# Kernel tuning notes

Measured on AMD Instinct MI355X. Metric: run time of the kernel, lower is better.

The kernel has to match this reference:

```python
import jax, jax.numpy as jnp
import numpy as np

N, E, F_IN, H, L, E_FEAT, G, OUT = 100000, 1600000, 8, 128, 4, 16, 256, 256


def setup_inputs() -> dict:
    key = jax.random.key(0)
    ks = jax.random.split(key, 12)
    inp = {
        "x": jax.random.normal(ks[0], (N, F_IN), jnp.float32),
        "edge_index": jax.random.randint(ks[1], (2, E), 0, N),
        "edge_attr": jax.random.uniform(ks[2], (E, E_FEAT), jnp.float32),
        "batch": jnp.sort(jax.random.randint(ks[3], (N,), 0, G)),
        "emb_W": jax.random.normal(ks[4], (F_IN, H), jnp.float32) / np.sqrt(F_IN),
        "emb_b": jnp.zeros((H,), jnp.float32),
        "edge_W": jax.random.normal(ks[5], (L, E_FEAT, H), jnp.float32) / np.sqrt(E_FEAT),
        "edge_b": jnp.zeros((L, H), jnp.float32),
        "nn_W": jax.random.normal(ks[6], (L, H, H), jnp.float32) / np.sqrt(H),
        "nn_b": jnp.zeros((L, H), jnp.float32),
        "bn_g": jnp.ones((L, H), jnp.float32),
        "bn_b": jnp.zeros((L, H), jnp.float32),
        "lin_W": jax.random.normal(ks[7], (H, OUT), jnp.float32) / np.sqrt(H),
        "lin_b": jnp.zeros((OUT,), jnp.float32),
    }
    return inp


def reference(x, edge_index, edge_attr, batch, emb_W, emb_b, edge_W, edge_b,
              nn_W, nn_b, bn_g, bn_b, lin_W, lin_b):
    eps_bn = 1e-5
    src, dst = edge_index[0], edge_index[1]
    h = x @ emb_W + emb_b  # node embedding [N,H]
    for l in range(L):
        e = edge_attr @ edge_W[l] + edge_b[l]          # [E,H] edge embedding
        msg = jax.nn.relu(h[src] + e)                   # gather + message
        agg = jax.ops.segment_sum(msg, dst, num_segments=N)  # scatter-add
        hc = (h + agg) @ nn_W[l] + nn_b[l]             # GINE nn (eps=0)
        mu = jnp.mean(hc, axis=0)
        var = jnp.mean((hc - mu) ** 2, axis=0)          # biased var (train BN)
        hc = (hc - mu) * jax.lax.rsqrt(var + eps_bn) * bn_g[l] + bn_b[l]
        hc = jax.nn.gelu(hc, approximate=False)
        h = h + hc                                      # 'res' residual
    out = h @ lin_W + lin_b                             # [N,OUT]
    rep = jax.ops.segment_sum(out, batch, num_segments=G)  # global_add_pool
    return rep
```

## Files before the change

kernel.cpp:

```cpp
#include <hip/hip_runtime.h>
#include <hip/hip_fp16.h>
#include <math.h>

#define GG 256

typedef __attribute__((ext_vector_type(8))) short short8;
typedef __attribute__((ext_vector_type(4))) float f32x4;
typedef _Float16 half4v __attribute__((ext_vector_type(4)));
typedef __attribute__((ext_vector_type(8))) unsigned uint8v;

__device__ __forceinline__ unsigned short f2bf(float x) {
  union { float f; unsigned u; } v; v.f = x;
  unsigned r = v.u + 0x7fff + ((v.u >> 16) & 1);
  return (unsigned short)(r >> 16);
}

__device__ __forceinline__ unsigned pack_h2(float a, float b) {
  __half2 h = __floats2half2_rn(a, b);
  return *(unsigned*)&h;
}

__device__ __forceinline__ uint8v sload8(const void* p) {
  uint8v r;
  asm volatile("s_load_dwordx8 %0, %1, 0x0"
               : "=s"(r) : "s"((unsigned long long)p));
  return r;
}
__device__ __forceinline__ void swait() {
  asm volatile("s_waitcnt lgkmcnt(0)" ::: "memory");
  __builtin_amdgcn_sched_barrier(0);
}

__global__ __launch_bounds__(256) void k_emb(const float* __restrict__ x,
    const float* __restrict__ W, const float* __restrict__ b,
    float* __restrict__ h, unsigned short* __restrict__ hb, int N) {
  int idx = blockIdx.x * 256 + threadIdx.x;
  if (idx >= N * 32) return;
  int n = idx >> 5, q = idx & 31;
  const float* xr = x + (size_t)n * 8;
  float xs[8];
#pragma unroll
  for (int k = 0; k < 8; ++k) xs[k] = xr[k];
  float4 acc = ((const float4*)b)[q];
#pragma unroll
  for (int k = 0; k < 8; ++k) {
    float4 w = ((const float4*)(W + (size_t)k * 128))[q];
    acc.x += xs[k] * w.x; acc.y += xs[k] * w.y;
    acc.z += xs[k] * w.z; acc.w += xs[k] * w.w;
  }
  ((float4*)h)[idx] = acc;
  ushort4 hv4 = make_ushort4(f2bf(acc.x), f2bf(acc.y), f2bf(acc.z), f2bf(acc.w));
  *(ushort4*)(hb + (size_t)idx * 4) = hv4;
}

__global__ __launch_bounds__(256) void k_wconv2(const float* __restrict__ eW,
    unsigned* __restrict__ eWf) {
  int i = blockIdx.x * 256 + threadIdx.x;
  if (i >= 2048) return;
  int lane = i & 63, nt = (i >> 6) & 7, l = i >> 9;
  int l15 = lane & 15, quad = lane >> 4;
  const float* base = eW + (size_t)l * 16 * 128 + (size_t)(nt * 16 + l15);
  unsigned lo = pack_h2(base[(quad * 4 + 0) * 128], base[(quad * 4 + 1) * 128]);
  unsigned hi = pack_h2(base[(quad * 4 + 2) * 128], base[(quad * 4 + 3) * 128]);
  eWf[(size_t)i * 2] = lo;
  eWf[(size_t)i * 2 + 1] = hi;
}

__global__ __launch_bounds__(256) void k_nnconv(const float* __restrict__ W,
    unsigned short* __restrict__ WT) {
  int i = blockIdx.x * 256 + threadIdx.x;
  if (i >= 4 * 128 * 128) return;
  int n = i & 127, k = (i >> 7) & 127, l = i >> 14;
  WT[((size_t)(l * 128 + n)) * 128 + k] = f2bf(W[i]);
}

__global__ void k_hist(const int* __restrict__ dst, int* __restrict__ deg, int E) {
  int e = blockIdx.x * blockDim.x + threadIdx.x;
  if (e < E) atomicAdd(&deg[dst[e]], 1);
}

__global__ __launch_bounds__(256) void k_scan_reduce(const int* __restrict__ deg,
    int* __restrict__ bsum, int N) {
  __shared__ int sd[256];
  int i = blockIdx.x * 256 + threadIdx.x;
  sd[threadIdx.x] = (i < N) ? deg[i] : 0;
  __syncthreads();
  for (int s = 128; s > 0; s >>= 1) {
    if (threadIdx.x < s) sd[threadIdx.x] += sd[threadIdx.x + s];
    __syncthreads();
  }
  if (threadIdx.x == 0) bsum[blockIdx.x] = sd[0];
}

__global__ __launch_bounds__(512) void k_scan_mid(int* bsum, int nb) {
  __shared__ int sd[512];
  int t = threadIdx.x;
  int v = (t < nb) ? bsum[t] : 0;
  sd[t] = v; __syncthreads();
  for (int d = 1; d < 512; d <<= 1) {
    int xv = (t >= d) ? sd[t - d] : 0;
    __syncthreads();
    sd[t] += xv;
    __syncthreads();
  }
  if (t < nb) bsum[t] = sd[t] - v;
}

__global__ __launch_bounds__(256) void k_scan_final(const int* __restrict__ deg,
    const int* __restrict__ bsum, int* __restrict__ offs,
    int* __restrict__ cursor, int N) {
  __shared__ int sd[256];
  int t = threadIdx.x;
  int i = blockIdx.x * 256 + t;
  int v = (i < N) ? deg[i] : 0;
  sd[t] = v; __syncthreads();
  for (int d = 1; d < 256; d <<= 1) {
    int xv = (t >= d) ? sd[t - d] : 0;
    __syncthreads();
    sd[t] += xv;
    __syncthreads();
  }
  int off = bsum[blockIdx.x] + sd[t] - v;
  if (i < N) {
    offs[i] = off; cursor[i] = off;
    if (i == N - 1) offs[N] = off + v;
  }
}

__global__ void k_fill(const int* __restrict__ src, const int* __restrict__ dst,
    const float* __restrict__ attr, int* __restrict__ cursor,
    int* __restrict__ csrc, uint4* __restrict__ cattr16, int E) {
  int e = blockIdx.x * blockDim.x + threadIdx.x;
  if (e >= E) return;
  int d = dst[e];
  int pos = atomicAdd(&cursor[d], 1);
  csrc[pos] = src[e];
  const float4* a = (const float4*)(attr + (size_t)e * 16);
  float4 a0 = a[0], a1 = a[1], a2 = a[2], a3 = a[3];
  uint4 o0, o1;
  o0.x = pack_h2(a0.x, a0.y); o0.y = pack_h2(a0.z, a0.w);
  o0.z = pack_h2(a1.x, a1.y); o0.w = pack_h2(a1.z, a1.w);
  o1.x = pack_h2(a2.x, a2.y); o1.y = pack_h2(a2.z, a2.w);
  o1.z = pack_h2(a3.x, a3.y); o1.w = pack_h2(a3.z, a3.w);
  cattr16[(size_t)pos * 2] = o0;
  cattr16[(size_t)pos * 2 + 1] = o1;
}

__global__ void k_gstart(const int* __restrict__ batch, int* __restrict__ gstart,
                         int N, int Gn) {
  int i = blockIdx.x * blockDim.x + threadIdx.x;
  if (i >= N) return;
  int b = batch[i];
  if (i == 0) { for (int g = 0; g <= b; ++g) gstart[g] = 0; }
  else { int bp = batch[i - 1]; for (int g = bp + 1; g <= b; ++g) gstart[g] = i; }
  if (i == N - 1) { for (int g = b + 1; g <= Gn; ++g) gstart[g] = N; }
}

__global__ __launch_bounds__(256) void k_edge_agg(const float* __restrict__ h,
    const unsigned* __restrict__ hb32,
    const uint4* __restrict__ cattr16, const int* __restrict__ csrc,
    const int* __restrict__ offs, const unsigned* __restrict__ eWf,
    const float* __restrict__ eb, unsigned* __restrict__ hpa16,
    float* __restrict__ cstats, int N) {
  __shared__ float elds_all[4][16 * 132];
  int t = threadIdx.x;
  if (blockIdx.x == 0) cstats[t] = 0.f;
  int lane = t & 63;
  int l15 = lane & 15, quad = lane >> 4;
  int wid = blockIdx.x * 4 + (t >> 6);
  int nw = gridDim.x * 4;
  float* elds = elds_all[t >> 6];
  uint2 bfr[8];
#pragma unroll
  for (int nt = 0; nt < 8; ++nt) bfr[nt] = ((const uint2*)eWf)[nt * 64 + lane];
  float2 bias = *(const float2*)(eb + 2 * lane);
  const unsigned* hb_l = hb32 + lane;

#define GI(r, SC)                                                           \
  unsigned u##r = 0;                                                        \
  if (j0 + (r) < je) u##r = hb_l[(size_t)(unsigned)(SC) * 64];

#define EPI(r, UU, AX, AY)                                                  \
  if (j0 + (r) < je) {                                                      \
    float2 ev = *(const float2*)&elds[(r) * 132 + 2 * lane];                \
    union { unsigned uu; float ff; } c0, c1;                                \
    c0.uu = (UU) << 16; c1.uu = (UU) & 0xffff0000u;                         \
    AX += fmaxf(ev.x + bias.x + c0.ff, 0.f);                                \
    AY += fmaxf(ev.y + bias.y + c1.ff, 0.f);                                \
  }

  for (int n = wid; n < N; n += nw) {
    int jb = __builtin_amdgcn_readfirstlane(offs[n]);
    int je = __builtin_amdgcn_readfirstlane(offs[n + 1]);
    float ax = 0.f, ay = 0.f, bx = 0.f, by = 0.f;
    for (int j0 = jb; j0 < je; j0 += 16) {
      uint8v scA = sload8((const char*)csrc + ((size_t)(unsigned)j0 << 2));
      uint8v scB = sload8((const char*)csrc + ((size_t)(unsigned)(j0 + 8) << 2));
      uint2 araw = *(const uint2*)((const char*)cattr16 +
                    ((size_t)(unsigned)(j0 + l15)) * 32 + quad * 8);
      swait();
      GI(0, scA[0]) GI(1, scA[1]) GI(2, scA[2]) GI(3, scA[3])
      GI(4, scA[4]) GI(5, scA[5]) GI(6, scA[6]) GI(7, scA[7])
      GI(8, scB[0]) GI(9, scB[1]) GI(10, scB[2]) GI(11, scB[3])
      GI(12, scB[4]) GI(13, scB[5]) GI(14, scB[6]) GI(15, scB[7])
      half4v av;
      __builtin_memcpy(&av, &araw, 8);
      f32x4 ee[8];
#pragma unroll
      for (int nt = 0; nt < 8; ++nt) {
        half4v bv;
        __builtin_memcpy(&bv, &bfr[nt], 8);
        ee[nt] = __builtin_amdgcn_mfma_f32_16x16x16f16(
            av, bv, (f32x4){0.f, 0.f, 0.f, 0.f}, 0, 0, 0);
      }
#pragma unroll
      for (int nt = 0; nt < 8; ++nt)
#pragma unroll
        for (int reg = 0; reg < 4; ++reg)
          elds[(quad * 4 + reg) * 132 + nt * 16 + l15] = ee[nt][reg];
      EPI(0, u0, ax, ay)  EPI(1, u1, bx, by)
      EPI(2, u2, ax, ay)  EPI(3, u3, bx, by)
      EPI(4, u4, ax, ay)  EPI(5, u5, bx, by)
      EPI(6, u6, ax, ay)  EPI(7, u7, bx, by)
      EPI(8, u8, ax, ay)  EPI(9, u9, bx, by)
      EPI(10, u10, ax, ay) EPI(11, u11, bx, by)
      EPI(12, u12, ax, ay) EPI(13, u13, bx, by)
      EPI(14, u14, ax, ay) EPI(15, u15, bx, by)
    }
    float2 hvv = *(const float2*)(h + (size_t)n * 128 + 2 * lane);
    float rx = hvv.x + ax + bx;
    float ry = hvv.y + ay + by;
    hpa16[(size_t)n * 64 + lane] = ((unsigned)f2bf(ry) << 16) | (unsigned)f2bf(rx);
  }
#undef GI
#undef EPI
}

__global__ __launch_bounds__(256) void k_gemm_mfma(
    const unsigned short* __restrict__ A16, const unsigned short* __restrict__ WT16,
    const float* __restrict__ bias, float* __restrict__ hc,
    float* __restrict__ cstats, int N) {
  __shared__ short a_lds[128 * 136];
  __shared__ short w_lds[128 * 136];
  int t = threadIdx.x;
  int rowbase = blockIdx.x * 128;
  {
    int r = t >> 1;
    int off = (t & 1) * 64;
    const short* ga = (const short*)A16 + (size_t)(rowbase + r) * 128 + off;
    short* la = &a_lds[r * 136 + off];
    const short* gw = (const short*)WT16 + (size_t)r * 128 + off;
    short* lw = &w_lds[r * 136 + off];
    if (rowbase + r < N) {
#pragma unroll
      for (int jj = 0; jj < 8; ++jj)
        *(uint4*)(la + jj * 8) = *(const uint4*)(ga + jj * 8);
    } else {
#pragma unroll
      for (int jj = 0; jj < 8; ++jj)
        *(uint4*)(la + jj * 8) = make_uint4(0, 0, 0, 0);
    }
#pragma unroll
    for (int jj = 0; jj < 8; ++jj)
      *(uint4*)(lw + jj * 8) = *(const uint4*)(gw + jj * 8);
  }
  __syncthreads();
  int w = t >> 6;
  int lane = t & 63;
  int l15 = lane & 15, quad = lane >> 4;
  f32x4 acc[2][8];
#pragma unroll
  for (int rt = 0; rt < 2; ++rt)
#pragma unroll
    for (int nt = 0; nt < 8; ++nt)
      acc[rt][nt] = (f32x4){0.f, 0.f, 0.f, 0.f};
#pragma unroll
  for (int kc = 0; kc < 4; ++kc) {
    int k0 = kc * 32 + quad * 8;
    short8 af0 = *(const short8*)&a_lds[(w * 32 + l15) * 136 + k0];
    short8 af1 = *(const short8*)&a_lds[(w * 32 + 16 + l15) * 136 + k0];
#pragma unroll
    for (int nt = 0; nt < 8; ++nt) {
      short8 bf = *(const short8*)&w_lds[(nt * 16 + l15) * 136 + k0];
      acc[0][nt] = __builtin_amdgcn_mfma_f32_16x16x32_bf16(af0, bf, acc[0][nt], 0, 0, 0);
      acc[1][nt] = __builtin_amdgcn_mfma_f32_16x16x32_bf16(af1, bf, acc[1][nt], 0, 0, 0);
    }
  }
  float sA[8], sQ[8];
#pragma unroll
  for (int nt = 0; nt < 8; ++nt) { sA[nt] = 0.f; sQ[nt] = 0.f; }
#pragma unroll
  for (int nt = 0; nt < 8; ++nt) {
    int col = nt * 16 + l15;
    float bv = bias[col];
#pragma unroll
    for (int rt = 0; rt < 2; ++rt) {
      int rbase = rowbase + w * 32 + rt * 16 + quad * 4;
#pragma unroll
      for (int reg = 0; reg < 4; ++reg) {
        int row = rbase + reg;
        float v = acc[rt][nt][reg] + bv;
        if (row < N) {
          hc[(size_t)row * 128 + col] = v;
          sA[nt] += v; sQ[nt] += v * v;
        }
      }
    }
  }
#pragma unroll
  for (int nt = 0; nt < 8; ++nt) {
    sA[nt] += __shfl_xor(sA[nt], 16);
    sA[nt] += __shfl_xor(sA[nt], 32);
    sQ[nt] += __shfl_xor(sQ[nt], 16);
    sQ[nt] += __shfl_xor(sQ[nt], 32);
  }
  __syncthreads();
  float* sdA = (float*)a_lds;
  float* sdQ = (float*)w_lds;
  if (quad == 0) {
#pragma unroll
    for (int nt = 0; nt < 8; ++nt) {
      sdA[w * 128 + nt * 16 + l15] = sA[nt];
      sdQ[w * 128 + nt * 16 + l15] = sQ[nt];
    }
  }
  __syncthreads();
  if (t < 128) {
    float s = sdA[t] + sdA[128 + t] + sdA[256 + t] + sdA[384 + t];
    float s2 = sdQ[t] + sdQ[128 + t] + sdQ[256 + t] + sdQ[384 + t];
    atomicAdd(&cstats[t], s);
    atomicAdd(&cstats[128 + t], s2);
  }
}

__global__ __launch_bounds__(256) void k_bn(const float* __restrict__ hc,
    const float* __restrict__ cstats,
    const float* __restrict__ g, const float* __restrict__ bb,
    float* __restrict__ h, unsigned short* __restrict__ hb, int N) {
  int idx = blockIdx.x * 256 + threadIdx.x;
  if (idx >= N * 32) return;
  int q = idx & 31;
  float invN = 1.f / (float)N;
  float4 cs = ((const float4*)cstats)[q];
  float4 cq = ((const float4*)cstats)[q + 32];
  float4 gv = ((const float4*)g)[q];
  float4 bv = ((const float4*)bb)[q];
  float4 v = ((const float4*)hc)[idx];
  float4 hv = ((const float4*)h)[idx];
#define BN1(X)                                                      \
  { float mu = cs.X * invN;                                         \
    float var = cq.X * invN - mu * mu;                              \
    float xn = (v.X - mu) * rsqrtf(var + 1e-5f) * gv.X + bv.X;      \
    hv.X += 0.5f * xn * (1.f + erff(xn * 0.70710678118654752f)); }
  BN1(x) BN1(y) BN1(z) BN1(w)
#undef BN1
  ((float4*)h)[idx] = hv;
  if (hb) {
    ushort4 hv4 = make_ushort4(f2bf(hv.x), f2bf(hv.y), f2bf(hv.z), f2bf(hv.w));
    *(ushort4*)(hb + (size_t)idx * 4) = hv4;
  }
}

__global__ __launch_bounds__(256) void k_poolfinal(const float* __restrict__ h,
    const int* __restrict__ gstart, const float* __restrict__ W,
    const float* __restrict__ b, float* __restrict__ out) {
  int g = blockIdx.x;
  int t = threadIdx.x, c = t & 127, half = t >> 7;
  int n0 = gstart[g], n1 = gstart[g + 1];
  float s = 0.f;
  for (int n = n0 + half; n < n1; n += 2) s += h[(size_t)n * 128 + c];
  __shared__ float ls[256];
  __shared__ float pr[128];
  ls[t] = s; __syncthreads();
  if (t < 128) pr[t] = ls[t] + ls[t + 128];
  __syncthreads();
  float cnt = (float)(n1 - n0);
  float acc = cnt * b[t];
#pragma unroll 8
  for (int k = 0; k < 128; ++k) acc += pr[k] * W[(size_t)k * 256 + t];
  out[(size_t)g * 256 + t] = acc;
}

extern "C" void kernel_launch(void* const* d_in, const int* in_sizes, int n_in,
                              void* d_out, int out_size, void* d_ws, size_t ws_size,
                              hipStream_t stream) {
  const float* x     = (const float*)d_in[0];
  const int*   eidx  = (const int*)d_in[1];
  const float* eattr = (const float*)d_in[2];
  const int*   batch = (const int*)d_in[3];
  const float* embW  = (const float*)d_in[4];
  const float* embB  = (const float*)d_in[5];
  const float* edgeW = (const float*)d_in[6];
  const float* edgeB = (const float*)d_in[7];
  const float* nnW   = (const float*)d_in[8];
  const float* nnB   = (const float*)d_in[9];
  const float* bnG   = (const float*)d_in[10];
  const float* bnB   = (const float*)d_in[11];
  const float* linW  = (const float*)d_in[12];
  const float* linB  = (const float*)d_in[13];
  float* out = (float*)d_out;

  int N = in_sizes[0] / 8;
  int E = in_sizes[1] / 2;
  const int* src = eidx;
  const int* dst = eidx + E;

  char* wptr = (char*)d_ws;
  auto alloc = [&](size_t bytes) {
    char* p = wptr; wptr += (bytes + 255) & ~(size_t)255; return p;
  };
  float* h      = (float*)alloc((size_t)N * 128 * 4);
  float* hc     = (float*)alloc((size_t)N * 128 * 4);
  unsigned short* hb = (unsigned short*)alloc((size_t)N * 128 * 2);
  unsigned* hpa16 = (unsigned*)alloc((size_t)N * 64 * 4);
  uint4* cattr16 = (uint4*)alloc((size_t)E * 32 + 1024);
  int*   csrc   = (int*)alloc((size_t)E * 4 + 256);
  int*   offs   = (int*)alloc((size_t)(N + 1) * 4);
  int*   cursor = (int*)alloc((size_t)N * 4);
  int*   deg    = (int*)alloc((size_t)N * 4);
  int nb = (N + 255) / 256;
  int*   bsum   = (int*)alloc((size_t)nb * 4);
  float* cstats = (float*)alloc(256 * 4);
  unsigned* eWf = (unsigned*)alloc(4096 * 4);
  unsigned short* WT16 = (unsigned short*)alloc(4 * 128 * 128 * 2);
  int*   gstart = (int*)alloc((size_t)(GG + 1) * 4);

  int q32 = (N * 32 + 255) / 256;

  hipMemsetAsync(deg, 0, (size_t)N * 4, stream);
  k_emb<<<q32, 256, 0, stream>>>(x, embW, embB, h, hb, N);
  k_wconv2<<<8, 256, 0, stream>>>(edgeW, eWf);
  k_nnconv<<<256, 256, 0, stream>>>(nnW, WT16);
  k_hist<<<(E + 255) / 256, 256, 0, stream>>>(dst, deg, E);
  k_scan_reduce<<<nb, 256, 0, stream>>>(deg, bsum, N);
  k_scan_mid<<<1, 512, 0, stream>>>(bsum, nb);
  k_scan_final<<<nb, 256, 0, stream>>>(deg, bsum, offs, cursor, N);
  k_fill<<<(E + 255) / 256, 256, 0, stream>>>(src, dst, eattr, cursor, csrc, cattr16, E);
  k_gstart<<<(N + 255) / 256, 256, 0, stream>>>(batch, gstart, N, GG);

  int gblk = (N + 127) / 128;
  for (int l = 0; l < 4; ++l) {
    k_edge_agg<<<8192, 256, 0, stream>>>(h, (const unsigned*)hb, cattr16, csrc,
        offs, eWf + (size_t)l * 1024, edgeB + (size_t)l * 128, hpa16, cstats, N);
    k_gemm_mfma<<<gblk, 256, 0, stream>>>((const unsigned short*)hpa16,
        WT16 + (size_t)l * 128 * 128, nnB + (size_t)l * 128, hc, cstats, N);
    k_bn<<<q32, 256, 0, stream>>>(hc, cstats,
        bnG + (size_t)l * 128, bnB + (size_t)l * 128, h, (l == 3) ? nullptr : hb, N);
  }
  k_poolfinal<<<GG, 256, 0, stream>>>(h, gstart, linW, linB, out);
}
```

Baseline: 1.064 ms.

## Prefetch next edge chunk indices and attrs; store edge embeddings as fp16 in LDS

Software-pipelines the per-node edge loop in the edge aggregation kernel. The scalar loads of the next 16 source indices and the next edge-attribute fragment are issued before the current chunk's MFMA and epilogue, so their latency overlaps with compute. It also halves the LDS staging of the MFMA edge embedding by storing fp16 instead of fp32. The cost is extra scalar registers and a loss of precision in the staged edge embeddings.

```diff
diff --git a/kernel.cpp b/kernel.cpp
--- a/kernel.cpp
+++ b/kernel.cpp
@@ -28,6 +28,10 @@
 }
 __device__ __forceinline__ void swait() {
   asm volatile("s_waitcnt lgkmcnt(0)" ::: "memory");
+  __builtin_amdgcn_sched_barrier(0);
+}
+__device__ __forceinline__ void swait2(uint8v& a, uint8v& b) {
+  asm volatile("s_waitcnt lgkmcnt(0)" : "+s"(a), "+s"(b) :: "memory");
   __builtin_amdgcn_sched_barrier(0);
 }
 
@@ -162,14 +166,14 @@
     const int* __restrict__ offs, const unsigned* __restrict__ eWf,
     const float* __restrict__ eb, unsigned* __restrict__ hpa16,
     float* __restrict__ cstats, int N) {
-  __shared__ float elds_all[4][16 * 132];
+  __shared__ __half elds_all[4][16 * 136];
   int t = threadIdx.x;
   if (blockIdx.x == 0) cstats[t] = 0.f;
   int lane = t & 63;
   int l15 = lane & 15, quad = lane >> 4;
   int wid = blockIdx.x * 4 + (t >> 6);
   int nw = gridDim.x * 4;
-  float* elds = elds_all[t >> 6];
+  __half* elds = elds_all[t >> 6];
   uint2 bfr[8];
 #pragma unroll
   for (int nt = 0; nt < 8; ++nt) bfr[nt] = ((const uint2*)eWf)[nt * 64 + lane];
@@ -182,50 +186,69 @@
 
 #define EPI(r, UU, AX, AY)                                                  \
   if (j0 + (r) < je) {                                                      \
-    float2 ev = *(const float2*)&elds[(r) * 132 + 2 * lane];                \
+    __half2 ev2 = *(__half2*)&elds[(r) * 136 + 2 * lane];                   \
     union { unsigned uu; float ff; } c0, c1;                                \
     c0.uu = (UU) << 16; c1.uu = (UU) & 0xffff0000u;                         \
-    AX += fmaxf(ev.x + bias.x + c0.ff, 0.f);                                \
-    AY += fmaxf(ev.y + bias.y + c1.ff, 0.f);                                \
-  }
+    AX += fmaxf(__low2float(ev2) + bias.x + c0.ff, 0.f);                    \
+    AY += fmaxf(__high2float(ev2) + bias.y + c1.ff, 0.f);                   \
+  }
+
+#define LOADA(DST, J0)                                                      \
+  DST = *(const uint2*)((const char*)cattr16 +                              \
+        ((size_t)(unsigned)((J0) + l15)) * 32 + quad * 8);
 
   for (int n = wid; n < N; n += nw) {
     int jb = __builtin_amdgcn_readfirstlane(offs[n]);
     int je = __builtin_amdgcn_readfirstlane(offs[n + 1]);
     float ax = 0.f, ay = 0.f, bx = 0.f, by = 0.f;
-    for (int j0 = jb; j0 < je; j0 += 16) {
-      uint8v scA = sload8((const char*)csrc + ((size_t)(unsigned)j0 << 2));
-      uint8v scB = sload8((const char*)csrc + ((size_t)(unsigned)(j0 + 8) << 2));
-      uint2 araw = *(const uint2*)((const char*)cattr16 +
-                    ((size_t)(unsigned)(j0 + l15)) * 32 + quad * 8);
-      swait();
-      GI(0, scA[0]) GI(1, scA[1]) GI(2, scA[2]) GI(3, scA[3])
-      GI(4, scA[4]) GI(5, scA[5]) GI(6, scA[6]) GI(7, scA[7])
-      GI(8, scB[0]) GI(9, scB[1]) GI(10, scB[2]) GI(11, scB[3])
-      GI(12, scB[4]) GI(13, scB[5]) GI(14, scB[6]) GI(15, scB[7])
-      half4v av;
-      __builtin_memcpy(&av, &araw, 8);
-      f32x4 ee[8];
-#pragma unroll
-      for (int nt = 0; nt < 8; ++nt) {
-        half4v bv;
-        __builtin_memcpy(&bv, &bfr[nt], 8);
-        ee[nt] = __builtin_amdgcn_mfma_f32_16x16x16f16(
-            av, bv, (f32x4){0.f, 0.f, 0.f, 0.f}, 0, 0, 0);
+    if (jb < je) {
+      uint8v scA = sload8((const char*)csrc + ((size_t)(unsigned)jb << 2));
+      uint8v scB = sload8((const char*)csrc + ((size_t)(unsigned)(jb + 8) << 2));
+      uint2 araw;
+      LOADA(araw, jb)
+      swait2(scA, scB);
+      for (int j0 = jb;;) {
+        GI(0, scA[0]) GI(1, scA[1]) GI(2, scA[2]) GI(3, scA[3])
+        GI(4, scA[4]) GI(5, scA[5]) GI(6, scA[6]) GI(7, scA[7])
+        GI(8, scB[0]) GI(9, scB[1]) GI(10, scB[2]) GI(11, scB[3])
+        GI(12, scB[4]) GI(13, scB[5]) GI(14, scB[6]) GI(15, scB[7])
+        bool more = (j0 + 16 < je);
+        uint8v scA2, scB2;
+        uint2 araw2;
+        if (more) {
+          scA2 = sload8((const char*)csrc + ((size_t)(unsigned)(j0 + 16) << 2));
+          scB2 = sload8((const char*)csrc + ((size_t)(unsigned)(j0 + 24) << 2));
+          LOADA(araw2, j0 + 16)
+        }
+        half4v av;
+        __builtin_memcpy(&av, &araw, 8);
+        f32x4 ee[8];
+#pragma unroll
+        for (int nt = 0; nt < 8; ++nt) {
+          half4v bv;
+          __builtin_memcpy(&bv, &bfr[nt], 8);
+          ee[nt] = __builtin_amdgcn_mfma_f32_16x16x16f16(
+              av, bv, (f32x4){0.f, 0.f, 0.f, 0.f}, 0, 0, 0);
+        }
+#pragma unroll
+        for (int nt = 0; nt < 8; ++nt)
+#pragma unroll
+          for (int reg = 0; reg < 4; ++reg)
+            elds[(quad * 4 + reg) * 136 + nt * 16 + l15] =
+                __float2half(ee[nt][reg]);
+        EPI(0, u0, ax, ay)  EPI(1, u1, bx, by)
+        EPI(2, u2, ax, ay)  EPI(3, u3, bx, by)
+        EPI(4, u4, ax, ay)  EPI(5, u5, bx, by)
+        EPI(6, u6, ax, ay)  EPI(7, u7, bx, by)
+        EPI(8, u8, ax, ay)  EPI(9, u9, bx, by)
+        EPI(10, u10, ax, ay) EPI(11, u11, bx, by)
+        EPI(12, u12, ax, ay) EPI(13, u13, bx, by)
+        EPI(14, u14, ax, ay) EPI(15, u15, bx, by)
+        j0 += 16;
+        if (!more) break;
+        swait2(scA2, scB2);
+        scA = scA2; scB = scB2; araw = araw2;
       }
-#pragma unroll
-      for (int nt = 0; nt < 8; ++nt)
-#pragma unroll
-        for (int reg = 0; reg < 4; ++reg)
-          elds[(quad * 4 + reg) * 132 + nt * 16 + l15] = ee[nt][reg];
-      EPI(0, u0, ax, ay)  EPI(1, u1, bx, by)
-      EPI(2, u2, ax, ay)  EPI(3, u3, bx, by)
-      EPI(4, u4, ax, ay)  EPI(5, u5, bx, by)
-      EPI(6, u6, ax, ay)  EPI(7, u7, bx, by)
-      EPI(8, u8, ax, ay)  EPI(9, u9, bx, by)
-      EPI(10, u10, ax, ay) EPI(11, u11, bx, by)
-      EPI(12, u12, ax, ay) EPI(13, u13, bx, by)
-      EPI(14, u14, ax, ay) EPI(15, u15, bx, by)
     }
     float2 hvv = *(const float2*)(h + (size_t)n * 128 + 2 * lane);
     float rx = hvv.x + ax + bx;
@@ -234,6 +257,7 @@
   }
 #undef GI
 #undef EPI
+#undef LOADA
 }
 
 __global__ __launch_bounds__(256) void k_gemm_mfma(
```

Measured after the change: 1.028 ms. -3.4%, faster.
